# Performance work log

Hardware: AMD Instinct MI355X
Metric: run time of the kernel (lower is better)

## Reference

```python
import jax, jax.numpy as jnp
import numpy as np

# norse.LIFCell default parameters
DT = 1e-3
TAU_SYN_INV = 200.0   # 1 / 5e-3
TAU_MEM_INV = 100.0   # 1 / 1e-2
V_TH = 1.0
V_LEAK = 0.0
V_RESET = 0.0
ALPHA = 100.0         # SuperSpike surrogate slope

T, B, N_IN, N_HIDDEN, N_OUT = 16, 4096, 784, 256, 10


@jax.custom_vjp
def heaviside(x):
    return (x > 0).astype(x.dtype)

def _h_fwd(x):
    return heaviside(x), x

def _h_bwd(x, g):
    # SuperSpike surrogate: d/dx H(x) ~ 1 / (alpha*|x| + 1)^2
    return (g / (ALPHA * jnp.abs(x) + 1.0) ** 2,)

heaviside.defvjp(_h_fwd, _h_bwd)


def lif_step(inp, v, i):
    """One norse lif_step: Euler-integrate v and i, spike, hard reset."""
    v_decayed = v + DT * TAU_MEM_INV * ((V_LEAK - v) + i)
    i_decayed = i - DT * TAU_SYN_INV * i
    z = heaviside(v_decayed - V_TH)
    v_new = (1.0 - z) * v_decayed + z * V_RESET
    i_new = i_decayed + inp
    return z, v_new, i_new


def setup_inputs() -> dict:
    key = jax.random.key(0)
    k1, k2, k3, k4, k5 = jax.random.split(key, 5)
    # binary spike trains (T, B, N_IN)
    spike_input = (jax.random.uniform(k1, (T, B, N_IN)) < 0.3).astype(jnp.float32)
    lim1 = float(1.0 / np.sqrt(N_IN))
    lim2 = float(1.0 / np.sqrt(N_HIDDEN))
    W1 = jax.random.uniform(k2, (N_HIDDEN, N_IN), minval=-lim1, maxval=lim1, dtype=jnp.float32)
    b1 = jax.random.uniform(k3, (N_HIDDEN,), minval=-lim1, maxval=lim1, dtype=jnp.float32)
    W2 = jax.random.uniform(k4, (N_OUT, N_HIDDEN), minval=-lim2, maxval=lim2, dtype=jnp.float32)
    b2 = jax.random.uniform(k5, (N_OUT,), minval=-lim2, maxval=lim2, dtype=jnp.float32)
    return {"spike_input": spike_input, "W1": W1, "b1": b1, "W2": W2, "b2": b2}


def reference(spike_input, W1, b1, W2, b2):
    batch = spike_input.shape[1]
    nh, no = W1.shape[0], W2.shape[0]
    dtype = spike_input.dtype
    # LIFCell with state=None starts at v=v_leak, i=0
    init = (jnp.full((batch, nh), V_LEAK, dtype), jnp.zeros((batch, nh), dtype),
            jnp.full((batch, no), V_LEAK, dtype), jnp.zeros((batch, no), dtype))

    def step(carry, x_t):
        v1, i1, v2, i2 = carry
        c1 = x_t @ W1.T + b1                 # (B, N_HIDDEN)
        z1, v1, i1 = lif_step(c1, v1, i1)
        c2 = z1 @ W2.T + b2                  # (B, N_OUT)
        z2, v2, i2 = lif_step(c2, v2, i2)
        return (v1, i1, v2, i2), z2

    _, zs = jax.lax.scan(step, init, spike_input)  # zs: (T, B, N_OUT)
    return zs.sum(axis=0)                          # (B, N_OUT)
```

## Files before the change

### kernel.cpp

```cpp
#include <hip/hip_runtime.h>


#define T_STEPS 16
#define B_SZ    4096
#define N_IN    784
#define N_HID   256
#define N_OUT   10
#define M_TOT   (T_STEPS * B_SZ)
#define KP8     832
#define WPLANE  (N_HID * KP8)
#define WROW    848
#define WPL     (16 * WROW)

typedef int    i32x4 __attribute__((ext_vector_type(4)));
typedef unsigned int u32;
typedef unsigned char u8;

__global__ __launch_bounds__(256) void conv_x(
    const float* __restrict__ X, u8* __restrict__ Xq)
{
    const long idx = (long)blockIdx.x * 256 + threadIdx.x;
    const long m = idx / 52;
    const int  s = (int)(idx - m * 52);
    uint4 o = make_uint4(0u, 0u, 0u, 0u);
    if (s < 49) {
        const uint4* src = reinterpret_cast<const uint4*>(X + m * N_IN + s * 16);
        const uint4 f0 = src[0], f1 = src[1], f2 = src[2], f3 = src[3];
        auto pk = [](uint4 f) -> u32 {
            return (f.x ? 1u : 0u) | ((f.y ? 1u : 0u) << 8) |
                   ((f.z ? 1u : 0u) << 16) | ((f.w ? 1u : 0u) << 24);
        };
        o.x = pk(f0); o.y = pk(f1); o.z = pk(f2); o.w = pk(f3);
    }
    reinterpret_cast<uint4*>(Xq)[idx] = o;
}

__global__ __launch_bounds__(256) void conv_w3(
    const float* __restrict__ W1, char* __restrict__ Wq)
{
    const int idx = blockIdx.x * 256 + threadIdx.x;
    if (idx >= N_HID * KP8) return;
    const int n = idx / KP8, k = idx % KP8;
    const float w = (k < N_IN) ? W1[n * N_IN + k] : 0.0f;
    const float a = rintf(w * 2048.0f);
    const float r1 = fmaf(a, -4.8828125e-4f, w);
    const float b = rintf(r1 * 262144.0f);
    const float r2 = fmaf(b, -3.814697265625e-6f, r1);
    const float c = rintf(r2 * 33554432.0f);
    Wq[idx]              = (char)(int)a;
    Wq[WPLANE + idx]     = (char)(int)b;
    Wq[2 * WPLANE + idx] = (char)(int)c;
}

__global__ __launch_bounds__(256, 2) void gemm1_lif1(
    const u8* __restrict__ Xq,
    const u8* __restrict__ Wq,
    const float* __restrict__ b1,
    u8* __restrict__ Z1)
{
    __shared__ u8 Bq[3 * WPL];

    const int tid  = threadIdx.x;
    const int lane = tid & 63;
    const int w    = tid >> 6;
    const int bid = blockIdx.x;
    const int l   = (bid & 7) * 64 + (bid >> 3);
    const int b0  = (l >> 4) * 128;
    const int n0  = (l & 15) * 16;
    const int ls  = lane >> 4;
    const int lr  = lane & 15;

    #pragma unroll
    for (int it = 0; it < 10; ++it) {
        const int u = it * 256 + tid;
        if (u < 2496) {
            const int plane = u / 832;
            const int rem   = u - plane * 832;
            const int row   = rem / 52;
            const int sp    = rem - row * 52;
            const uint4 v = *reinterpret_cast<const uint4*>(
                Wq + (size_t)plane * WPLANE + (size_t)(n0 + row) * KP8 + sp * 16);
            *reinterpret_cast<uint4*>(&Bq[plane * WPL + row * WROW + sp * 16]) = v;
        }
    }
    __syncthreads();

    const float bb = b1[n0 + lr];
    float vS[8], cS[8];
    #pragma unroll
    for (int k = 0; k < 8; ++k) { vS[k] = 0.0f; cS[k] = 0.0f; }

    int bO[3];
    #pragma unroll
    for (int p = 0; p < 3; ++p) bO[p] = p * WPL + lr * WROW + (ls << 4);

    const u8* aP0 = Xq + (size_t)(b0 + w * 32 + lr) * KP8 + ls * 16;
    const u8* aP1 = aP0 + 16 * KP8;
    const size_t TSTR = (size_t)B_SZ * KP8;

    const float s1 = 4.8828125e-4f;
    const float s2 = 3.814697265625e-6f;
    const float s3 = 2.9802322387695312e-8f;

    for (int t = 0; t < T_STEPS; ++t) {
        i32x4 acc[2][3];
        #pragma unroll
        for (int i = 0; i < 2; ++i)
            #pragma unroll
            for (int p = 0; p < 3; ++p)
                acc[i][p] = (i32x4){0, 0, 0, 0};

        uint4 ab[2][2];
        ab[0][0] = *reinterpret_cast<const uint4*>(aP0);
        ab[0][1] = *reinterpret_cast<const uint4*>(aP1);

        #pragma unroll
        for (int s = 0; s < 13; ++s) {
            const int cb = s & 1;
            if (s < 12) {
                ab[cb ^ 1][0] = *reinterpret_cast<const uint4*>(aP0 + (s + 1) * 64);
                ab[cb ^ 1][1] = *reinterpret_cast<const uint4*>(aP1 + (s + 1) * 64);
            }
            uint4 bf[3];
            #pragma unroll
            for (int p = 0; p < 3; ++p)
                bf[p] = *reinterpret_cast<const uint4*>(&Bq[bO[p] + s * 64]);
            #pragma unroll
            for (int i = 0; i < 2; ++i)
                #pragma unroll
                for (int p = 0; p < 3; ++p)
                    acc[i][p] = __builtin_amdgcn_mfma_i32_16x16x64_i8(
                        __builtin_bit_cast(i32x4, ab[cb][i]),
                        __builtin_bit_cast(i32x4, bf[p]),
                        acc[i][p], 0, 0, 0);
        }
        aP0 += TSTR; aP1 += TSTR;

        #pragma unroll
        for (int i = 0; i < 2; ++i) {
            #pragma unroll
            for (int q = 0; q < 4; ++q) {
                const int k = i * 4 + q;
                const float c1 = fmaf(s1, (float)acc[i][0][q],
                                 fmaf(s2, (float)acc[i][1][q],
                                 fmaf(s3, (float)acc[i][2][q], bb)));
                const float vd = vS[k] + 0.1f * ((0.0f - vS[k]) + cS[k]);
                const float id = cS[k] - 0.2f * cS[k];
                const bool  sp = vd > 1.0f;
                Z1[(size_t)(t * B_SZ + b0 + w * 32 + i * 16 + ls * 4 + q) * N_HID
                   + n0 + lr] = sp ? (u8)1 : (u8)0;
                vS[k] = sp ? 0.0f : vd;
                cS[k] = id + c1;
            }
        }
    }
}

__global__ __launch_bounds__(640) void gemm2_f32(
    const u8* __restrict__ Z, const float* __restrict__ W2,
    const float* __restrict__ b2, float* __restrict__ C2)
{
    __shared__ float zs[64 * 268];
    __shared__ float ws[N_OUT * N_HID];
    const int tid = threadIdx.x;
    const int m0 = blockIdx.x * 64;

    for (int c = tid; c < 1024; c += 640) {
        const int r = c >> 4;
        const int col = (c & 15) * 16;
        const uint4 v = *reinterpret_cast<const uint4*>(
            Z + (size_t)(m0 + r) * N_HID + col);
        float* d = &zs[r * 268 + col];
        const u32 wd[4] = {v.x, v.y, v.z, v.w};
        #pragma unroll
        for (int k = 0; k < 4; ++k)
            #pragma unroll
            for (int b = 0; b < 4; ++b)
                d[k * 4 + b] = (float)((wd[k] >> (8 * b)) & 0xffu);
    }
    *(float4*)&ws[tid * 4] = *(const float4*)&W2[tid * 4];
    __syncthreads();

    const int o = tid >> 6;
    const int r = tid & 63;
    float acc = b2[o];
    #pragma unroll
    for (int k = 0; k < N_HID; k += 4) {
        const float4 z4 = *(const float4*)&zs[r * 268 + k];
        const float4 w4 = *(const float4*)&ws[o * N_HID + k];
        acc += z4.x * w4.x + z4.y * w4.y + z4.z * w4.z + z4.w * w4.w;
    }
    C2[(size_t)(m0 + r) * N_OUT + o] = acc;
}

__global__ __launch_bounds__(256) void lif2_kernel(
    const float* __restrict__ C2, float* __restrict__ out)
{
    const int g = blockIdx.x * 256 + threadIdx.x;
    const int stride = B_SZ * N_OUT;
    float v = 0.0f, cur = 0.0f, s = 0.0f;
    #pragma unroll
    for (int t = 0; t < T_STEPS; ++t) {
        const float c = C2[t * stride + g];
        const float vd = v + 0.1f * ((0.0f - v) + cur);
        const float id = cur - 0.2f * cur;
        const bool  sp = vd > 1.0f;
        s += sp ? 1.0f : 0.0f;
        v = sp ? 0.0f : vd;
        cur = id + c;
    }
    out[g] = s;
}

extern "C" void kernel_launch(void* const* d_in, const int* in_sizes, int n_in,
                              void* d_out, int out_size, void* d_ws, size_t ws_size,
                              hipStream_t stream)
{
    const float* X  = (const float*)d_in[0];
    const float* W1 = (const float*)d_in[1];
    const float* b1 = (const float*)d_in[2];
    const float* W2 = (const float*)d_in[3];
    const float* b2 = (const float*)d_in[4];
    float* out = (float*)d_out;

    char* Wq = (char*)d_ws;
    u8*   Xq = (u8*)d_ws + (1 << 20);
    u8*   Z1 = Xq + (size_t)M_TOT * KP8;
    float* C2 = (float*)(Z1 + (size_t)M_TOT * N_HID);

    conv_x<<<(M_TOT * (KP8 / 16)) / 256, 256, 0, stream>>>(X, Xq);

    conv_w3<<<(N_HID * KP8) / 256, 256, 0, stream>>>(W1, Wq);

    gemm1_lif1<<<512, 256, 0, stream>>>(Xq, (const u8*)Wq, b1, Z1);

    gemm2_f32<<<M_TOT / 64, 640, 0, stream>>>(Z1, W2, b2, C2);

    lif2_kernel<<<(B_SZ * N_OUT) / 256, 256, 0, stream>>>(C2, out);
}
```

Before: 131.1 us.

## Batch four timesteps per GEMM pass to reuse LDS weight fragments

The gemm1 main loop now processes four timesteps together. Each weight fragment read from LDS feeds 24 MFMAs instead of 6, and the loads of four timesteps of X are in flight at once. This cuts LDS read traffic and gives more memory-level parallelism on the global X loads. The cost is many more live registers (96 accumulator VGPRs plus 16 uint4 prefetch buffers) with launch_bounds(256,2), which risks spills or lower occupancy.

```diff
diff --git a/kernel.cpp b/kernel.cpp
--- a/kernel.cpp
+++ b/kernel.cpp
@@ -94,63 +94,85 @@
     #pragma unroll
     for (int p = 0; p < 3; ++p) bO[p] = p * WPL + lr * WROW + (ls << 4);
 
+    const size_t TSTR = (size_t)B_SZ * KP8;
     const u8* aP0 = Xq + (size_t)(b0 + w * 32 + lr) * KP8 + ls * 16;
     const u8* aP1 = aP0 + 16 * KP8;
-    const size_t TSTR = (size_t)B_SZ * KP8;
 
     const float s1 = 4.8828125e-4f;
     const float s2 = 3.814697265625e-6f;
     const float s3 = 2.9802322387695312e-8f;
 
-    for (int t = 0; t < T_STEPS; ++t) {
-        i32x4 acc[2][3];
-        #pragma unroll
-        for (int i = 0; i < 2; ++i)
+    for (int g = 0; g < 4; ++g) {
+        i32x4 acc[4][2][3];
+        #pragma unroll
+        for (int tt = 0; tt < 4; ++tt)
+            #pragma unroll
+            for (int i = 0; i < 2; ++i)
+                #pragma unroll
+                for (int p = 0; p < 3; ++p)
+                    acc[tt][i][p] = (i32x4){0, 0, 0, 0};
+
+        uint4 ab[2][4][2];
+        #pragma unroll
+        for (int tt = 0; tt < 4; ++tt) {
+            const u8* p0 = aP0 + (size_t)tt * TSTR;
+            const u8* p1 = aP1 + (size_t)tt * TSTR;
+            ab[0][tt][0] = *reinterpret_cast<const uint4*>(p0);
+            ab[0][tt][1] = *reinterpret_cast<const uint4*>(p1);
+            ab[1][tt][0] = *reinterpret_cast<const uint4*>(p0 + 64);
+            ab[1][tt][1] = *reinterpret_cast<const uint4*>(p1 + 64);
+        }
+
+        #pragma unroll
+        for (int j = 0; j < 13; ++j) {
+            const int pb = j & 1;
+            uint4 bf[3];
             #pragma unroll
             for (int p = 0; p < 3; ++p)
-                acc[i][p] = (i32x4){0, 0, 0, 0};
-
-        uint4 ab[2][2];
-        ab[0][0] = *reinterpret_cast<const uint4*>(aP0);
-        ab[0][1] = *reinterpret_cast<const uint4*>(aP1);
-
-        #pragma unroll
-        for (int s = 0; s < 13; ++s) {
-            const int cb = s & 1;
-            if (s < 12) {
-                ab[cb ^ 1][0] = *reinterpret_cast<const uint4*>(aP0 + (s + 1) * 64);
-                ab[cb ^ 1][1] = *reinterpret_cast<const uint4*>(aP1 + (s + 1) * 64);
+                bf[p] = *reinterpret_cast<const uint4*>(&Bq[bO[p] + j * 64]);
+
+            #pragma unroll
+            for (int tt = 0; tt < 4; ++tt)
+                #pragma unroll
+                for (int i = 0; i < 2; ++i)
+                    #pragma unroll
+                    for (int p = 0; p < 3; ++p)
+                        acc[tt][i][p] = __builtin_amdgcn_mfma_i32_16x16x64_i8(
+                            __builtin_bit_cast(i32x4, ab[pb][tt][i]),
+                            __builtin_bit_cast(i32x4, bf[p]),
+                            acc[tt][i][p], 0, 0, 0);
+
+            if (j < 11) {
+                #pragma unroll
+                for (int tt = 0; tt < 4; ++tt) {
+                    const u8* p0 = aP0 + (size_t)tt * TSTR + (j + 2) * 64;
+                    const u8* p1 = aP1 + (size_t)tt * TSTR + (j + 2) * 64;
+                    ab[pb][tt][0] = *reinterpret_cast<const uint4*>(p0);
+                    ab[pb][tt][1] = *reinterpret_cast<const uint4*>(p1);
+                }
             }
-            uint4 bf[3];
-            #pragma unroll
-            for (int p = 0; p < 3; ++p)
-                bf[p] = *reinterpret_cast<const uint4*>(&Bq[bO[p] + s * 64]);
-            #pragma unroll
-            for (int i = 0; i < 2; ++i)
-                #pragma unroll
-                for (int p = 0; p < 3; ++p)
-                    acc[i][p] = __builtin_amdgcn_mfma_i32_16x16x64_i8(
-                        __builtin_bit_cast(i32x4, ab[cb][i]),
-                        __builtin_bit_cast(i32x4, bf[p]),
-                        acc[i][p], 0, 0, 0);
-        }
-        aP0 += TSTR; aP1 += TSTR;
-
-        #pragma unroll
-        for (int i = 0; i < 2; ++i) {
-            #pragma unroll
-            for (int q = 0; q < 4; ++q) {
-                const int k = i * 4 + q;
-                const float c1 = fmaf(s1, (float)acc[i][0][q],
-                                 fmaf(s2, (float)acc[i][1][q],
-                                 fmaf(s3, (float)acc[i][2][q], bb)));
-                const float vd = vS[k] + 0.1f * ((0.0f - vS[k]) + cS[k]);
-                const float id = cS[k] - 0.2f * cS[k];
-                const bool  sp = vd > 1.0f;
-                Z1[(size_t)(t * B_SZ + b0 + w * 32 + i * 16 + ls * 4 + q) * N_HID
-                   + n0 + lr] = sp ? (u8)1 : (u8)0;
-                vS[k] = sp ? 0.0f : vd;
-                cS[k] = id + c1;
+        }
+        aP0 += 4 * TSTR; aP1 += 4 * TSTR;
+
+        #pragma unroll
+        for (int tt = 0; tt < 4; ++tt) {
+            const int t = 4 * g + tt;
+            #pragma unroll
+            for (int i = 0; i < 2; ++i) {
+                #pragma unroll
+                for (int q = 0; q < 4; ++q) {
+                    const int k = i * 4 + q;
+                    const float c1 = fmaf(s1, (float)acc[tt][i][0][q],
+                                     fmaf(s2, (float)acc[tt][i][1][q],
+                                     fmaf(s3, (float)acc[tt][i][2][q], bb)));
+                    const float vd = vS[k] + 0.1f * ((0.0f - vS[k]) + cS[k]);
+                    const float id = cS[k] - 0.2f * cS[k];
+                    const bool  sp = vd > 1.0f;
+                    Z1[(size_t)(t * B_SZ + b0 + w * 32 + i * 16 + ls * 4 + q) * N_HID
+                       + n0 + lr] = sp ? (u8)1 : (u8)0;
+                    vS[k] = sp ? 0.0f : vd;
+                    cS[k] = id + c1;
+                }
             }
         }
     }
```

Measured after the change: 202.7 us. +54.6%, slower.
